# Kernel tuning notes

Hardware: AMD Instinct MI355X
Metric: run time of the kernel (lower is better)

Reference implementation:

```python
import jax, jax.numpy as jnp
import numpy as np

N_NODES = 50000
N_EDGES = 1600000
IN_CH = 256
ADAPTER = 64
EDGE_DIM = 32


def setup_inputs() -> dict:
    key = jax.random.key(0)
    ks = jax.random.split(key, 12)
    s = lambda k, shape: jax.random.normal(k, shape, dtype=jnp.float32) * 0.05
    x = jax.random.normal(ks[0], (N_NODES, IN_CH), dtype=jnp.float32)
    edge_index = jax.random.randint(ks[1], (2, N_EDGES), 0, N_NODES, dtype=jnp.int64)
    edge_attr = jax.random.normal(ks[2], (N_EDGES, EDGE_DIM), dtype=jnp.float32)
    return {
        "x": x,
        "edge_index": edge_index,
        "edge_attr": edge_attr,
        "W_down": s(ks[3], (ADAPTER, IN_CH)),
        "b_down": jnp.zeros((ADAPTER,), jnp.float32),
        "W_time": s(ks[4], (ADAPTER, EDGE_DIM)),
        "b_time": jnp.zeros((ADAPTER,), jnp.float32),
        "W_fusion": s(ks[5], (ADAPTER, 2 * ADAPTER)),
        "b_fusion": jnp.zeros((ADAPTER,), jnp.float32),
        "W_up": s(ks[6], (IN_CH, ADAPTER)),
        "b_up": jnp.zeros((IN_CH,), jnp.float32),
    }


def reference(x, edge_index, edge_attr, W_down, b_down, W_time, b_time,
              W_fusion, b_fusion, W_up, b_up):
    n = x.shape[0]
    # down-projection + ReLU: [N, adapter]
    node_feat = jax.nn.relu(x @ W_down.T + b_down)
    # time projection + ReLU: [E, adapter]
    time_feat = jax.nn.relu(edge_attr @ W_time.T + b_time)
    # scatter_mean over source nodes (edge_index[0]) -> [N, adapter]
    src = edge_index[0]
    sums = jax.ops.segment_sum(time_feat, src, num_segments=n)
    counts = jax.ops.segment_sum(jnp.ones((time_feat.shape[0],), jnp.float32), src,
                                 num_segments=n)
    node_time_feat = sums / jnp.maximum(counts, 1.0)[:, None]
    # fuse + ReLU + up-projection + residual
    combined = jnp.concatenate([node_feat, node_time_feat], axis=-1)
    fused = jax.nn.relu(combined @ W_fusion.T + b_fusion)
    out = fused @ W_up.T + b_up
    return x + out
```

## Files before the change

kernel.cpp:

```cpp
#include <hip/hip_runtime.h>

#define N_NODES 50000
#define N_EDGES 1600000
#define IN_CH   256
#define ADP     64
#define EDGE_DIM 32
#define GRP     196
#define GCAP    12288
#define EPB_A   2048
#define NB_BUCKET ((N_EDGES + EPB_A - 1) / EPB_A)
#define NT16    (N_NODES / 16)
#define NB_GEMM ((NT16 + 3) / 4)

typedef __fp16 h2 __attribute__((ext_vector_type(2)));
typedef _Float16 f16x8 __attribute__((ext_vector_type(8)));
typedef float f32x4 __attribute__((ext_vector_type(4)));
union F8 { f16x8 v; h2 h[4]; };

__device__ inline f16x8 cvt8(float4 a, float4 b) {
    F8 r;
    r.h[0] = __builtin_amdgcn_cvt_pkrtz(a.x, a.y);
    r.h[1] = __builtin_amdgcn_cvt_pkrtz(a.z, a.w);
    r.h[2] = __builtin_amdgcn_cvt_pkrtz(b.x, b.y);
    r.h[3] = __builtin_amdgcn_cvt_pkrtz(b.z, b.w);
    return r.v;
}

__global__ __launch_bounds__(256) void k_bucket(const int* __restrict__ ei_src,
                                                int* __restrict__ gcnt,
                                                int* __restrict__ gbuf) {
    __shared__ int cnt[GRP];
    __shared__ int cur[GRP];
    int t = threadIdx.x;
    if (t < GRP) cnt[t] = 0;
    __syncthreads();
    int base = blockIdx.x * EPB_A;
    int s[8];
    #pragma unroll
    for (int k = 0; k < 8; k++) {
        int e = base + k * 256 + t;
        int v = (e < N_EDGES) ? ei_src[e] : -1;
        s[k] = v;
        if (v >= 0) atomicAdd(&cnt[v >> 8], 1);
    }
    __syncthreads();
    if (t < GRP) cur[t] = atomicAdd(&gcnt[t], cnt[t]);
    __syncthreads();
    #pragma unroll
    for (int k = 0; k < 8; k++) {
        int v = s[k];
        if (v >= 0) {
            int e = base + k * 256 + t;
            int g = v >> 8;
            int slot = atomicAdd(&cur[g], 1);
            if (slot < GCAP)
                gbuf[g * GCAP + slot] = (e << 8) | (v & 255);
        }
    }
}

__global__ __launch_bounds__(512) void k_build(const int* __restrict__ gcnt,
                                               const int* __restrict__ gbuf,
                                               int* __restrict__ deg,
                                               int* __restrict__ offs,
                                               int* __restrict__ elist) {
    __shared__ int a[256], b[256], dcnt[256], cur[256];
    int t = threadIdx.x;
    int g = blockIdx.x;
    if (t < 256) a[t] = (t < GRP) ? min(gcnt[t], GCAP) : 0;
    __syncthreads();
    int* sp = a; int* dp = b;
    for (int o = 1; o < 256; o <<= 1) {
        if (t < 256) { int v2 = sp[t]; if (t >= o) v2 += sp[t - o]; dp[t] = v2; }
        __syncthreads();
        int* tmp = sp; sp = dp; dp = tmp;
    }
    int base = (g == 0) ? 0 : sp[g - 1];
    int sz = min(gcnt[g], GCAP);
    if (t < 256) dcnt[t] = 0;
    __syncthreads();
    const int* src = gbuf + (size_t)g * GCAP;
    for (int i = t; i < sz; i += 512) atomicAdd(&dcnt[src[i] & 255], 1);
    __syncthreads();
    if (t < 256) a[t] = dcnt[t];
    __syncthreads();
    sp = a; dp = b;
    for (int o = 1; o < 256; o <<= 1) {
        if (t < 256) { int v2 = sp[t]; if (t >= o) v2 += sp[t - o]; dp[t] = v2; }
        __syncthreads();
        int* tmp = sp; sp = dp; dp = tmp;
    }
    if (t < 256) {
        int v = dcnt[t];
        int pref = sp[t] - v;
        int n = g * 256 + t;
        if (n < N_NODES) { deg[n] = v; offs[n] = base + pref; }
        cur[t] = pref;
    }
    __syncthreads();
    for (int i = t; i < sz; i += 512) {
        int p = src[i];
        int slot = atomicAdd(&cur[p & 255], 1);
        elist[base + slot] = p >> 8;
    }
}

__global__ __launch_bounds__(256) void k_gatherproj(const float* __restrict__ ea,
                                                    const int* __restrict__ offs,
                                                    const int* __restrict__ deg,
                                                    const int* __restrict__ elist,
                                                    const float* __restrict__ Wt,
                                                    const float* __restrict__ bt,
                                                    float* __restrict__ ntf) {
    int t = threadIdx.x;
    int lane = t & 63;
    int col = lane & 15, q = lane >> 4;
    f16x8 bf[4];
    float bias[4];
    #pragma unroll
    for (int nt = 0; nt < 4; nt++) {
        const float4* wr = (const float4*)(Wt + (size_t)(nt * 16 + col) * EDGE_DIM + q * 8);
        bf[nt] = cvt8(wr[0], wr[1]);
        bias[nt] = bt[nt * 16 + col];
    }
    int n = blockIdx.x * 4 + (t >> 6);
    if (n >= N_NODES) return;
    int st = offs[n], d = deg[n];
    const float4* ea4 = (const float4*)ea;
    float s0 = 0.f, s1 = 0.f, s2 = 0.f, s3 = 0.f;
    f32x4 z = {0.f, 0.f, 0.f, 0.f};
    int base = 0;
    for (; base + 32 <= d; base += 32) {
        int e0 = elist[st + base + col];
        int e1 = elist[st + base + 16 + col];
        const float4* p0 = ea4 + (size_t)e0 * 8 + q * 2;
        const float4* p1 = ea4 + (size_t)e1 * 8 + q * 2;
        float4 va0 = p0[0], va1 = p0[1];
        float4 vb0 = p1[0], vb1 = p1[1];
        f16x8 afA = cvt8(va0, va1);
        f16x8 afB = cvt8(vb0, vb1);
        f32x4 dA0 = __builtin_amdgcn_mfma_f32_16x16x32_f16(afA, bf[0], z, 0, 0, 0);
        f32x4 dA1 = __builtin_amdgcn_mfma_f32_16x16x32_f16(afA, bf[1], z, 0, 0, 0);
        f32x4 dA2 = __builtin_amdgcn_mfma_f32_16x16x32_f16(afA, bf[2], z, 0, 0, 0);
        f32x4 dA3 = __builtin_amdgcn_mfma_f32_16x16x32_f16(afA, bf[3], z, 0, 0, 0);
        f32x4 dB0 = __builtin_amdgcn_mfma_f32_16x16x32_f16(afB, bf[0], z, 0, 0, 0);
        f32x4 dB1 = __builtin_amdgcn_mfma_f32_16x16x32_f16(afB, bf[1], z, 0, 0, 0);
        f32x4 dB2 = __builtin_amdgcn_mfma_f32_16x16x32_f16(afB, bf[2], z, 0, 0, 0);
        f32x4 dB3 = __builtin_amdgcn_mfma_f32_16x16x32_f16(afB, bf[3], z, 0, 0, 0);
        #pragma unroll
        for (int r = 0; r < 4; r++) {
            s0 += fmaxf(dA0[r] + bias[0], 0.f) + fmaxf(dB0[r] + bias[0], 0.f);
            s1 += fmaxf(dA1[r] + bias[1], 0.f) + fmaxf(dB1[r] + bias[1], 0.f);
            s2 += fmaxf(dA2[r] + bias[2], 0.f) + fmaxf(dB2[r] + bias[2], 0.f);
            s3 += fmaxf(dA3[r] + bias[3], 0.f) + fmaxf(dB3[r] + bias[3], 0.f);
        }
    }
    for (; base < d; base += 16) {
        int cnt = d - base; if (cnt > 16) cnt = 16;
        int e = elist[st + base + (col < cnt ? col : cnt - 1)];
        const float4* p = ea4 + (size_t)e * 8 + q * 2;
        float4 v0 = p[0], v1 = p[1];
        f16x8 af = cvt8(v0, v1);
        f32x4 d0 = __builtin_amdgcn_mfma_f32_16x16x32_f16(af, bf[0], z, 0, 0, 0);
        f32x4 d1 = __builtin_amdgcn_mfma_f32_16x16x32_f16(af, bf[1], z, 0, 0, 0);
        f32x4 d2 = __builtin_amdgcn_mfma_f32_16x16x32_f16(af, bf[2], z, 0, 0, 0);
        f32x4 d3 = __builtin_amdgcn_mfma_f32_16x16x32_f16(af, bf[3], z, 0, 0, 0);
        #pragma unroll
        for (int r = 0; r < 4; r++) {
            bool ok = (q * 4 + r) < cnt;
            s0 += ok ? fmaxf(d0[r] + bias[0], 0.f) : 0.f;
            s1 += ok ? fmaxf(d1[r] + bias[1], 0.f) : 0.f;
            s2 += ok ? fmaxf(d2[r] + bias[2], 0.f) : 0.f;
            s3 += ok ? fmaxf(d3[r] + bias[3], 0.f) : 0.f;
        }
    }
    s0 += __shfl_xor(s0, 16, 64); s0 += __shfl_xor(s0, 32, 64);
    s1 += __shfl_xor(s1, 16, 64); s1 += __shfl_xor(s1, 32, 64);
    s2 += __shfl_xor(s2, 16, 64); s2 += __shfl_xor(s2, 32, 64);
    s3 += __shfl_xor(s3, 16, 64); s3 += __shfl_xor(s3, 32, 64);
    float res = (q == 0) ? s0 : (q == 1) ? s1 : (q == 2) ? s2 : s3;
    ntf[(size_t)n * ADP + lane] = res / fmaxf((float)d, 1.f);
}

__global__ __launch_bounds__(256) void k_down(const float* __restrict__ x,
                                              const float* __restrict__ Wd,
                                              const float* __restrict__ bd,
                                              float* __restrict__ nfeat) {
    __shared__ f16x8 wlds[8][4][64];
    int t = threadIdx.x;
    int lane = t & 63, col = lane & 15, q = lane >> 4;
    for (int f = t; f < 8 * 4 * 64; f += 256) {
        int l = f & 63, ntk = f >> 6;
        int nt = ntk & 3, kc = ntk >> 2;
        const float4* wr = (const float4*)(Wd + (size_t)(nt * 16 + (l & 15)) * IN_CH
                                           + kc * 32 + (l >> 4) * 8);
        wlds[kc][nt][l] = cvt8(wr[0], wr[1]);
    }
    __syncthreads();
    int tile = blockIdx.x * 4 + (t >> 6);
    if (tile >= NT16) return;
    int n0 = tile * 16;
    float bias[4];
    #pragma unroll
    for (int nt = 0; nt < 4; nt++) bias[nt] = bd[nt * 16 + col];
    f32x4 z = {0.f, 0.f, 0.f, 0.f};
    f32x4 acc[4];
    #pragma unroll
    for (int nt = 0; nt < 4; nt++) acc[nt] = z;
    #pragma unroll
    for (int kc = 0; kc < 8; kc++) {
        const float4* xr = (const float4*)(x + (size_t)(n0 + col) * IN_CH + kc * 32 + q * 8);
        float4 v0 = xr[0], v1 = xr[1];
        f16x8 af = cvt8(v0, v1);
        #pragma unroll
        for (int nt = 0; nt < 4; nt++)
            acc[nt] = __builtin_amdgcn_mfma_f32_16x16x32_f16(af, wlds[kc][nt][lane], acc[nt], 0, 0, 0);
    }
    #pragma unroll
    for (int nt = 0; nt < 4; nt++)
        #pragma unroll
        for (int r = 0; r < 4; r++)
            nfeat[(size_t)(n0 + q * 4 + r) * ADP + nt * 16 + col] = fmaxf(acc[nt][r] + bias[nt], 0.f);
}

__global__ __launch_bounds__(256) void k_fuse(const float* __restrict__ nfeat,
                                              const float* __restrict__ ntf,
                                              const float* __restrict__ Wf,
                                              const float* __restrict__ bf_,
                                              float* __restrict__ fused) {
    __shared__ f16x8 wlds[4][4][64];
    int t = threadIdx.x;
    int lane = t & 63, col = lane & 15, q = lane >> 4;
    for (int f = t; f < 4 * 4 * 64; f += 256) {
        int l = f & 63, ntk = f >> 6;
        int nt = ntk & 3, kc = ntk >> 2;
        const float4* wr = (const float4*)(Wf + (size_t)(nt * 16 + (l & 15)) * (2 * ADP)
                                           + kc * 32 + (l >> 4) * 8);
        wlds[kc][nt][l] = cvt8(wr[0], wr[1]);
    }
    __syncthreads();
    int tile = blockIdx.x * 4 + (t >> 6);
    if (tile >= NT16) return;
    int n0 = tile * 16;
    float bias[4];
    #pragma unroll
    for (int nt = 0; nt < 4; nt++) bias[nt] = bf_[nt * 16 + col];
    f32x4 z = {0.f, 0.f, 0.f, 0.f};
    f32x4 acc[4];
    #pragma unroll
    for (int nt = 0; nt < 4; nt++) acc[nt] = z;
    #pragma unroll
    for (int kc = 0; kc < 4; kc++) {
        const float* srcb = (kc < 2) ? nfeat : ntf;
        int ko = (kc & 1) * 32;
        const float4* xr = (const float4*)(srcb + (size_t)(n0 + col) * ADP + ko + q * 8);
        float4 v0 = xr[0], v1 = xr[1];
        f16x8 af = cvt8(v0, v1);
        #pragma unroll
        for (int nt = 0; nt < 4; nt++)
            acc[nt] = __builtin_amdgcn_mfma_f32_16x16x32_f16(af, wlds[kc][nt][lane], acc[nt], 0, 0, 0);
    }
    #pragma unroll
    for (int nt = 0; nt < 4; nt++)
        #pragma unroll
        for (int r = 0; r < 4; r++)
            fused[(size_t)(n0 + q * 4 + r) * ADP + nt * 16 + col] = fmaxf(acc[nt][r] + bias[nt], 0.f);
}

__global__ __launch_bounds__(256) void k_up(const float* __restrict__ fused,
                                            const float* __restrict__ x,
                                            const float* __restrict__ Wu,
                                            const float* __restrict__ bu,
                                            float* __restrict__ out) {
    __shared__ f16x8 wlds[2][16][64];
    int t = threadIdx.x;
    int lane = t & 63, col = lane & 15, q = lane >> 4;
    for (int f = t; f < 2 * 16 * 64; f += 256) {
        int l = f & 63, ntk = f >> 6;
        int nt = ntk & 15, kc = ntk >> 4;
        const float4* wr = (const float4*)(Wu + (size_t)(nt * 16 + (l & 15)) * ADP
                                           + kc * 32 + (l >> 4) * 8);
        wlds[kc][nt][l] = cvt8(wr[0], wr[1]);
    }
    __syncthreads();
    int tile = blockIdx.x * 4 + (t >> 6);
    if (tile >= NT16) return;
    int n0 = tile * 16;
    f32x4 z = {0.f, 0.f, 0.f, 0.f};
    f32x4 acc[16];
    #pragma unroll
    for (int nt = 0; nt < 16; nt++) acc[nt] = z;
    #pragma unroll
    for (int kc = 0; kc < 2; kc++) {
        const float4* xr = (const float4*)(fused + (size_t)(n0 + col) * ADP + kc * 32 + q * 8);
        float4 v0 = xr[0], v1 = xr[1];
        f16x8 af = cvt8(v0, v1);
        #pragma unroll
        for (int nt = 0; nt < 16; nt++)
            acc[nt] = __builtin_amdgcn_mfma_f32_16x16x32_f16(af, wlds[kc][nt][lane], acc[nt], 0, 0, 0);
    }
    #pragma unroll
    for (int nt = 0; nt < 16; nt++) {
        float b = bu[nt * 16 + col];
        #pragma unroll
        for (int r = 0; r < 4; r++) {
            size_t idx = (size_t)(n0 + q * 4 + r) * IN_CH + nt * 16 + col;
            out[idx] = x[idx] + acc[nt][r] + b;
        }
    }
}

extern "C" void kernel_launch(void* const* d_in, const int* in_sizes, int n_in,
                              void* d_out, int out_size, void* d_ws, size_t ws_size,
                              hipStream_t stream) {
    const float* x   = (const float*)d_in[0];
    const int*   ei  = (const int*)d_in[1];
    const float* ea  = (const float*)d_in[2];
    const float* Wd  = (const float*)d_in[3];
    const float* bd  = (const float*)d_in[4];
    const float* Wt  = (const float*)d_in[5];
    const float* bt  = (const float*)d_in[6];
    const float* Wf  = (const float*)d_in[7];
    const float* bf  = (const float*)d_in[8];
    const float* Wu  = (const float*)d_in[9];
    const float* bu  = (const float*)d_in[10];
    float* out = (float*)d_out;

    int* deg    = (int*)d_ws;
    int* offs   = deg + N_NODES;
    int* gcnt   = offs + N_NODES;
    int* elist  = gcnt + 256;
    float* ntf   = (float*)(elist + N_EDGES);
    float* nfeat = ntf + (size_t)N_NODES * ADP;
    float* fused = nfeat + (size_t)N_NODES * ADP;
    int* gbuf = (int*)nfeat;

    (void)hipMemsetAsync(gcnt, 0, 256 * sizeof(int), stream);

    k_bucket    <<<NB_BUCKET, 256, 0, stream>>>(ei, gcnt, gbuf);
    k_build     <<<     GRP, 512, 0, stream>>>(gcnt, gbuf, deg, offs, elist);
    k_gatherproj<<<   12500, 256, 0, stream>>>(ea, offs, deg, elist, Wt, bt, ntf);
    k_down      <<< NB_GEMM, 256, 0, stream>>>(x, Wd, bd, nfeat);
    k_fuse      <<< NB_GEMM, 256, 0, stream>>>(nfeat, ntf, Wf, bf, fused);
    k_up        <<< NB_GEMM, 256, 0, stream>>>(fused, x, Wu, bu, out);
}
```

Before: 479.0 us.

## Bucket fp16 edge payloads by node group and accumulate in LDS

The bucketing kernel now copies each edge's attributes, converted to fp16, into per-group contiguous buffers along with a 16-bit local node id. This replaces the CSR build and the random per-edge gather. A new per-group kernel runs the MFMA time projection over these contiguous payloads and scatter-adds the ReLU outputs and counts into an LDS accumulator, then writes the means. The goal is to drop the k_build pass and the uncoalesced edge_attr gathers. The costs are a larger write in the bucket pass, LDS float atomics with possible contention, and only 196 blocks in the accumulate kernel, which limits parallelism.

```diff
diff --git a/kernel.cpp b/kernel.cpp
--- a/kernel.cpp
+++ b/kernel.cpp
@@ -15,10 +15,10 @@
 typedef __fp16 h2 __attribute__((ext_vector_type(2)));
 typedef _Float16 f16x8 __attribute__((ext_vector_type(8)));
 typedef float f32x4 __attribute__((ext_vector_type(4)));
-union F8 { f16x8 v; h2 h[4]; };
+union UH { unsigned int u; h2 h; };
 
 __device__ inline f16x8 cvt8(float4 a, float4 b) {
-    F8 r;
+    union { f16x8 v; h2 h[4]; } r;
     r.h[0] = __builtin_amdgcn_cvt_pkrtz(a.x, a.y);
     r.h[1] = __builtin_amdgcn_cvt_pkrtz(a.z, a.w);
     r.h[2] = __builtin_amdgcn_cvt_pkrtz(b.x, b.y);
@@ -26,9 +26,20 @@
     return r.v;
 }
 
+__device__ inline uint4 pack8(float4 a, float4 b) {
+    UH p0, p1, p2, p3;
+    p0.h = __builtin_amdgcn_cvt_pkrtz(a.x, a.y);
+    p1.h = __builtin_amdgcn_cvt_pkrtz(a.z, a.w);
+    p2.h = __builtin_amdgcn_cvt_pkrtz(b.x, b.y);
+    p3.h = __builtin_amdgcn_cvt_pkrtz(b.z, b.w);
+    return make_uint4(p0.u, p1.u, p2.u, p3.u);
+}
+
 __global__ __launch_bounds__(256) void k_bucket(const int* __restrict__ ei_src,
+                                                const float* __restrict__ ea,
                                                 int* __restrict__ gcnt,
-                                                int* __restrict__ gbuf) {
+                                                _Float16* __restrict__ payload,
+                                                unsigned short* __restrict__ nid) {
     __shared__ int cnt[GRP];
     __shared__ int cur[GRP];
     int t = threadIdx.x;
@@ -49,72 +60,36 @@
     #pragma unroll
     for (int k = 0; k < 8; k++) {
         int v = s[k];
-        if (v >= 0) {
-            int e = base + k * 256 + t;
-            int g = v >> 8;
-            int slot = atomicAdd(&cur[g], 1);
-            if (slot < GCAP)
-                gbuf[g * GCAP + slot] = (e << 8) | (v & 255);
-        }
-    }
-}
-
-__global__ __launch_bounds__(512) void k_build(const int* __restrict__ gcnt,
-                                               const int* __restrict__ gbuf,
-                                               int* __restrict__ deg,
-                                               int* __restrict__ offs,
-                                               int* __restrict__ elist) {
-    __shared__ int a[256], b[256], dcnt[256], cur[256];
-    int t = threadIdx.x;
-    int g = blockIdx.x;
-    if (t < 256) a[t] = (t < GRP) ? min(gcnt[t], GCAP) : 0;
-    __syncthreads();
-    int* sp = a; int* dp = b;
-    for (int o = 1; o < 256; o <<= 1) {
-        if (t < 256) { int v2 = sp[t]; if (t >= o) v2 += sp[t - o]; dp[t] = v2; }
-        __syncthreads();
-        int* tmp = sp; sp = dp; dp = tmp;
-    }
-    int base = (g == 0) ? 0 : sp[g - 1];
-    int sz = min(gcnt[g], GCAP);
+        if (v < 0) continue;
+        int e = base + k * 256 + t;
+        int g = v >> 8;
+        int slot = atomicAdd(&cur[g], 1);
+        if (slot >= GCAP) continue;
+        size_t sb = (size_t)g * GCAP + slot;
+        nid[sb] = (unsigned short)(v & 255);
+        const float4* er = (const float4*)(ea + (size_t)e * EDGE_DIM);
+        float4 a0 = er[0], a1 = er[1], a2 = er[2], a3 = er[3];
+        float4 a4 = er[4], a5 = er[5], a6 = er[6], a7 = er[7];
+        uint4* dst = (uint4*)(payload + sb * EDGE_DIM);
+        dst[0] = pack8(a0, a1);
+        dst[1] = pack8(a2, a3);
+        dst[2] = pack8(a4, a5);
+        dst[3] = pack8(a6, a7);
+    }
+}
+
+__global__ __launch_bounds__(256) void k_accum(const int* __restrict__ gcnt,
+                                               const _Float16* __restrict__ payload,
+                                               const unsigned short* __restrict__ nid,
+                                               const float* __restrict__ Wt,
+                                               const float* __restrict__ bt,
+                                               float* __restrict__ ntf) {
+    __shared__ float accs[256 * 65];
+    __shared__ int dcnt[256];
+    int t = threadIdx.x;
+    int lane = t & 63, wv = t >> 6, col = lane & 15, q = lane >> 4;
+    for (int i = t; i < 256 * 65; i += 256) accs[i] = 0.f;
     if (t < 256) dcnt[t] = 0;
-    __syncthreads();
-    const int* src = gbuf + (size_t)g * GCAP;
-    for (int i = t; i < sz; i += 512) atomicAdd(&dcnt[src[i] & 255], 1);
-    __syncthreads();
-    if (t < 256) a[t] = dcnt[t];
-    __syncthreads();
-    sp = a; dp = b;
-    for (int o = 1; o < 256; o <<= 1) {
-        if (t < 256) { int v2 = sp[t]; if (t >= o) v2 += sp[t - o]; dp[t] = v2; }
-        __syncthreads();
-        int* tmp = sp; sp = dp; dp = tmp;
-    }
-    if (t < 256) {
-        int v = dcnt[t];
-        int pref = sp[t] - v;
-        int n = g * 256 + t;
-        if (n < N_NODES) { deg[n] = v; offs[n] = base + pref; }
-        cur[t] = pref;
-    }
-    __syncthreads();
-    for (int i = t; i < sz; i += 512) {
-        int p = src[i];
-        int slot = atomicAdd(&cur[p & 255], 1);
-        elist[base + slot] = p >> 8;
-    }
-}
-
-__global__ __launch_bounds__(256) void k_gatherproj(const float* __restrict__ ea,
-                                                    const int* __restrict__ offs,
-                                                    const int* __restrict__ deg,
-                                                    const int* __restrict__ elist,
-                                                    const float* __restrict__ Wt,
-                                                    const float* __restrict__ bt,
-                                                    float* __restrict__ ntf) {
-    int t = threadIdx.x;
-    int lane = t & 63;
-    int col = lane & 15, q = lane >> 4;
     f16x8 bf[4];
     float bias[4];
     #pragma unroll
@@ -123,63 +98,42 @@
         bf[nt] = cvt8(wr[0], wr[1]);
         bias[nt] = bt[nt * 16 + col];
     }
-    int n = blockIdx.x * 4 + (t >> 6);
-    if (n >= N_NODES) return;
-    int st = offs[n], d = deg[n];
-    const float4* ea4 = (const float4*)ea;
-    float s0 = 0.f, s1 = 0.f, s2 = 0.f, s3 = 0.f;
-    f32x4 z = {0.f, 0.f, 0.f, 0.f};
-    int base = 0;
-    for (; base + 32 <= d; base += 32) {
-        int e0 = elist[st + base + col];
-        int e1 = elist[st + base + 16 + col];
-        const float4* p0 = ea4 + (size_t)e0 * 8 + q * 2;
-        const float4* p1 = ea4 + (size_t)e1 * 8 + q * 2;
-        float4 va0 = p0[0], va1 = p0[1];
-        float4 vb0 = p1[0], vb1 = p1[1];
-        f16x8 afA = cvt8(va0, va1);
-        f16x8 afB = cvt8(vb0, vb1);
-        f32x4 dA0 = __builtin_amdgcn_mfma_f32_16x16x32_f16(afA, bf[0], z, 0, 0, 0);
-        f32x4 dA1 = __builtin_amdgcn_mfma_f32_16x16x32_f16(afA, bf[1], z, 0, 0, 0);
-        f32x4 dA2 = __builtin_amdgcn_mfma_f32_16x16x32_f16(afA, bf[2], z, 0, 0, 0);
-        f32x4 dA3 = __builtin_amdgcn_mfma_f32_16x16x32_f16(afA, bf[3], z, 0, 0, 0);
-        f32x4 dB0 = __builtin_amdgcn_mfma_f32_16x16x32_f16(afB, bf[0], z, 0, 0, 0);
-        f32x4 dB1 = __builtin_amdgcn_mfma_f32_16x16x32_f16(afB, bf[1], z, 0, 0, 0);
-        f32x4 dB2 = __builtin_amdgcn_mfma_f32_16x16x32_f16(afB, bf[2], z, 0, 0, 0);
-        f32x4 dB3 = __builtin_amdgcn_mfma_f32_16x16x32_f16(afB, bf[3], z, 0, 0, 0);
-        #pragma unroll
-        for (int r = 0; r < 4; r++) {
-            s0 += fmaxf(dA0[r] + bias[0], 0.f) + fmaxf(dB0[r] + bias[0], 0.f);
-            s1 += fmaxf(dA1[r] + bias[1], 0.f) + fmaxf(dB1[r] + bias[1], 0.f);
-            s2 += fmaxf(dA2[r] + bias[2], 0.f) + fmaxf(dB2[r] + bias[2], 0.f);
-            s3 += fmaxf(dA3[r] + bias[3], 0.f) + fmaxf(dB3[r] + bias[3], 0.f);
-        }
-    }
-    for (; base < d; base += 16) {
-        int cnt = d - base; if (cnt > 16) cnt = 16;
-        int e = elist[st + base + (col < cnt ? col : cnt - 1)];
-        const float4* p = ea4 + (size_t)e * 8 + q * 2;
-        float4 v0 = p[0], v1 = p[1];
-        f16x8 af = cvt8(v0, v1);
+    __syncthreads();
+    int g = blockIdx.x;
+    int sz = min(gcnt[g], GCAP);
+    const _Float16* pl = payload + (size_t)g * GCAP * EDGE_DIM;
+    const unsigned short* nd = nid + (size_t)g * GCAP;
+    f32x4 z = {0.f, 0.f, 0.f, 0.f};
+    for (int i0 = wv * 16; i0 < sz; i0 += 64) {
+        int cnt_b = min(16, sz - i0);
+        int ecol = col < cnt_b ? col : cnt_b - 1;
+        f16x8 af = *(const f16x8*)(pl + (size_t)(i0 + ecol) * EDGE_DIM + q * 8);
         f32x4 d0 = __builtin_amdgcn_mfma_f32_16x16x32_f16(af, bf[0], z, 0, 0, 0);
         f32x4 d1 = __builtin_amdgcn_mfma_f32_16x16x32_f16(af, bf[1], z, 0, 0, 0);
         f32x4 d2 = __builtin_amdgcn_mfma_f32_16x16x32_f16(af, bf[2], z, 0, 0, 0);
         f32x4 d3 = __builtin_amdgcn_mfma_f32_16x16x32_f16(af, bf[3], z, 0, 0, 0);
         #pragma unroll
         for (int r = 0; r < 4; r++) {
-            bool ok = (q * 4 + r) < cnt;
-            s0 += ok ? fmaxf(d0[r] + bias[0], 0.f) : 0.f;
-            s1 += ok ? fmaxf(d1[r] + bias[1], 0.f) : 0.f;
-            s2 += ok ? fmaxf(d2[r] + bias[2], 0.f) : 0.f;
-            s3 += ok ? fmaxf(d3[r] + bias[3], 0.f) : 0.f;
+            int er = q * 4 + r;
+            if (er < cnt_b) {
+                int node = nd[i0 + er];
+                float* row = &accs[node * 65];
+                atomicAdd(&row[col],      fmaxf(d0[r] + bias[0], 0.f));
+                atomicAdd(&row[16 + col], fmaxf(d1[r] + bias[1], 0.f));
+                atomicAdd(&row[32 + col], fmaxf(d2[r] + bias[2], 0.f));
+                atomicAdd(&row[48 + col], fmaxf(d3[r] + bias[3], 0.f));
+                if (col == 0) atomicAdd(&dcnt[node], 1);
+            }
         }
     }
-    s0 += __shfl_xor(s0, 16, 64); s0 += __shfl_xor(s0, 32, 64);
-    s1 += __shfl_xor(s1, 16, 64); s1 += __shfl_xor(s1, 32, 64);
-    s2 += __shfl_xor(s2, 16, 64); s2 += __shfl_xor(s2, 32, 64);
-    s3 += __shfl_xor(s3, 16, 64); s3 += __shfl_xor(s3, 32, 64);
-    float res = (q == 0) ? s0 : (q == 1) ? s1 : (q == 2) ? s2 : s3;
-    ntf[(size_t)n * ADP + lane] = res / fmaxf((float)d, 1.f);
+    __syncthreads();
+    int gn0 = g * 256;
+    for (int idx = t; idx < 256 * 64; idx += 256) {
+        int nl = idx >> 6, ch = idx & 63;
+        int n = gn0 + nl;
+        if (n < N_NODES)
+            ntf[(size_t)n * ADP + ch] = accs[nl * 65 + ch] / fmaxf((float)dcnt[nl], 1.f);
+    }
 }
 
 __global__ __launch_bounds__(256) void k_down(const float* __restrict__ x,
@@ -326,21 +280,18 @@
     const float* bu  = (const float*)d_in[10];
     float* out = (float*)d_out;
 
-    int* deg    = (int*)d_ws;
-    int* offs   = deg + N_NODES;
-    int* gcnt   = offs + N_NODES;
-    int* elist  = gcnt + 256;
-    float* ntf   = (float*)(elist + N_EDGES);
+    int* gcnt = (int*)d_ws;
+    unsigned short* nid = (unsigned short*)(gcnt + 256);
+    float* ntf   = (float*)(nid + (size_t)GRP * GCAP);
     float* nfeat = ntf + (size_t)N_NODES * ADP;
     float* fused = nfeat + (size_t)N_NODES * ADP;
-    int* gbuf = (int*)nfeat;
+    _Float16* payload = (_Float16*)(fused + (size_t)N_NODES * ADP);
 
     (void)hipMemsetAsync(gcnt, 0, 256 * sizeof(int), stream);
 
-    k_bucket    <<<NB_BUCKET, 256, 0, stream>>>(ei, gcnt, gbuf);
-    k_build     <<<     GRP, 512, 0, stream>>>(gcnt, gbuf, deg, offs, elist);
-    k_gatherproj<<<   12500, 256, 0, stream>>>(ea, offs, deg, elist, Wt, bt, ntf);
-    k_down      <<< NB_GEMM, 256, 0, stream>>>(x, Wd, bd, nfeat);
-    k_fuse      <<< NB_GEMM, 256, 0, stream>>>(nfeat, ntf, Wf, bf, fused);
-    k_up        <<< NB_GEMM, 256, 0, stream>>>(fused, x, Wu, bu, out);
-}
+    k_bucket<<<NB_BUCKET, 256, 0, stream>>>(ei, ea, gcnt, payload, nid);
+    k_accum <<<     GRP, 256, 0, stream>>>(gcnt, payload, nid, Wt, bt, ntf);
+    k_down  <<< NB_GEMM, 256, 0, stream>>>(x, Wd, bd, nfeat);
+    k_fuse  <<< NB_GEMM, 256, 0, stream>>>(nfeat, ntf, Wf, bf, fused);
+    k_up    <<< NB_GEMM, 256, 0, stream>>>(fused, x, Wu, bu, out);
+}
```

After: 1.157 ms. 142% more time.
